# Kernel tuning notes

Hardware: AMD Instinct MI355X
Metric: run time of the kernel (lower is better)

## Reference

```python
import jax, jax.numpy as jnp
import numpy as np

DT = 0.1
WHEELBASE = 2.8
STATE_DIM = 12


def setup_inputs() -> dict:
    key = jax.random.key(0)
    k1, k2, k3 = jax.random.split(key, 3)
    b, l, h = 512, 64, 80
    x0 = jax.random.normal(k1, (b, STATE_DIM), dtype=jnp.float32)
    controls = jax.random.normal(k2, (b, l, h, 3), dtype=jnp.float32)
    deg = jax.random.uniform(k3, (b, 5), dtype=jnp.float32)
    return {"x0": x0, "controls": controls, "deg": deg}


def reference(x0, controls, deg):
    b, l, h, _ = controls.shape
    # degradation scales, broadcast over the l (candidate) dim: [b, 1]
    steer_scale = jnp.maximum(deg[:, 0:1], 0.05)
    brake_scale = jnp.maximum(deg[:, 1:2], 0.05)
    throttle_scale = jnp.maximum(deg[:, 2:3], 0.05)
    friction = jnp.maximum(deg[:, 4:5], 0.1)

    x_init = jnp.broadcast_to(x0[:, None, :], (b, l, x0.shape[-1]))  # [b,l,12]

    def step(x, u):  # x: [b,l,12], u: [b,l,3]
        delta = steer_scale * jnp.tanh(u[..., 0])
        fb = brake_scale * jax.nn.sigmoid(u[..., 1])
        fx = throttle_scale * jax.nn.sigmoid(u[..., 2])
        px, py, psi, vx, vy = (x[..., 0], x[..., 1], x[..., 2], x[..., 3], x[..., 4])
        speed = jnp.sqrt(vx * vx + vy * vy + 1e-06)
        acc = jnp.minimum(jnp.maximum(2.8 * fx - 6.5 * fb, -7.5 * friction), 3.0)
        speed2 = jnp.maximum(speed + acc * DT, 0.0)
        tan_d = jnp.tan(jnp.clip(delta, -0.75, 0.75))
        raw_yaw = speed2 / WHEELBASE * tan_d
        yaw_lim = jnp.maximum(friction * 9.81 / jnp.maximum(speed2, 2.0), 0.15)
        yaw_rate = jnp.clip(raw_yaw, -1.0, 1.0) * yaw_lim
        beta = jnp.clip(jnp.arctan(0.45 * tan_d), -0.65, 0.65)
        psi2 = psi + yaw_rate * DT
        vx2 = speed2 * jnp.cos(psi2 + beta)
        vy2 = speed2 * jnp.sin(psi2 + beta)
        px2 = px + vx2 * DT
        py2 = py + vy2 * DT
        ax = (vx2 - vx) / DT
        ay = (vy2 - vy) / DT
        x2 = jnp.stack([px2, py2, psi2, vx2, vy2, yaw_rate, ax, ay, beta, delta, fb, fx], -1)
        return x2, x2

    controls_t = jnp.moveaxis(controls, 2, 0)  # [h,b,l,3]
    _, traj = jax.lax.scan(step, x_init, controls_t)  # traj: [h,b,l,12]
    traj = jnp.concatenate([x_init[None], traj], axis=0)  # [h+1,b,l,12]
    return jnp.moveaxis(traj, 0, 2)  # [b,l,h+1,12]
```

## Files before the change

kernel.cpp:

```cpp
#include <hip/hip_runtime.h>
#include <math.h>


#define N_B 512
#define N_L 64
#define N_H 80
#define DT_F 0.1f
#define PITCH_F4 25
#define SPC 8
#define NCH 10
#define INV2PI 0.15915494309189535f

__device__ __forceinline__ float fast_rcp(float x) { return __builtin_amdgcn_rcpf(x); }

__device__ __forceinline__ float fast_tanh(float x) {
    const float e2 = __expf(2.0f * x);
    return (e2 - 1.0f) * fast_rcp(e2 + 1.0f);
}

__device__ __forceinline__ float fast_sigmoid(float x) {
    return fast_rcp(1.0f + __expf(-x));
}

__device__ __forceinline__ float fast_atan_small(float z) {
    const float z2 = z * z;
    float p = 1.0f / 9.0f;
    p = fmaf(p, z2, -1.0f / 7.0f);
    p = fmaf(p, z2, 1.0f / 5.0f);
    p = fmaf(p, z2, -1.0f / 3.0f);
    p = fmaf(p, z2, 1.0f);
    return z * p;
}

struct Ctl { float delta, fb, fx, tan_d, beta, acc; };

__device__ __forceinline__ Ctl make_ctl(float u0, float u1, float u2,
                                        float steer_scale, float brake_scale,
                                        float throttle_scale, float neg_brake_lim) {
    Ctl t;
    t.delta = steer_scale * fast_tanh(u0);
    t.fb = brake_scale    * fast_sigmoid(u1);
    t.fx = throttle_scale * fast_sigmoid(u2);
    const float dc = fminf(fmaxf(t.delta, -0.75f), 0.75f);
    const float dr = dc * INV2PI;
    const float sd = __builtin_amdgcn_sinf(dr);
    const float cd = __builtin_amdgcn_cosf(dr);
    t.tan_d = sd * fast_rcp(cd);
    t.beta = fminf(fmaxf(fast_atan_small(0.45f * t.tan_d), -0.65f), 0.65f);
    t.acc = fminf(fmaxf(2.8f * t.fx - 6.5f * t.fb, neg_brake_lim), 3.0f);
    return t;
}

__global__ __launch_bounds__(128) void degraded_bicycle_rollout_kernel(
    const float* __restrict__ x0,
    const float* __restrict__ controls,
    const float* __restrict__ deg,
    float* __restrict__ out)
{
    __shared__ float4 lds4[2][N_L * PITCH_F4];

    const int lane = threadIdx.x & 63;
    const int wave = threadIdx.x >> 6;
    const int b = blockIdx.x;

    const size_t out_b = (size_t)b * 62208;

#define FLUSH_SLICE(FBUF, FC, I0, I1)                                             \
    {                                                                             \
        const size_t obase = out_b + 12 + (size_t)(FC) * (SPC * 12);              \
        _Pragma("unroll")                                                         \
        for (int i = (I0); i < (I1); ++i) {                                       \
            const unsigned flat = i * 64 + lane;                                  \
            const unsigned l = flat / 24u;                                        \
            const unsigned q = flat - l * 24u;                                    \
            const float4 v = lds4[FBUF][l * PITCH_F4 + q];                        \
            *reinterpret_cast<float4*>(out + obase + (size_t)l * 972 + q * 4) = v;\
        }                                                                         \
    }

    if (wave == 0) {
        const float* dg = deg + b * 5;
        const float steer_scale    = fmaxf(dg[0], 0.05f);
        const float brake_scale    = fmaxf(dg[1], 0.05f);
        const float throttle_scale = fmaxf(dg[2], 0.05f);
        const float friction       = fmaxf(dg[4], 0.1f);

        const float4* x0v = reinterpret_cast<const float4*>(x0 + b * 12);
        const float4 xi0 = x0v[0];
        const float4 xi1 = x0v[1];

        float px  = xi0.x;
        float py  = xi0.y;
        float psi = xi0.z;
        float vx  = xi0.w;
        float vy  = xi1.x;

        const int tid = b * 64 + lane;
        const float4* uc = reinterpret_cast<const float4*>(controls + (size_t)tid * 240);

        const float neg_brake_lim = -7.5f * friction;
        const float yaw_num = friction * 9.81f;
        const float inv_wheelbase = 1.0f / 2.8f;

        float4 c0 = uc[0];
        float4 c1 = uc[1];
        float4 c2 = uc[2];

        for (int c = 0; c < NCH; ++c) {
            float4* lrow = &lds4[c & 1][lane * PITCH_F4];

            #pragma unroll
            for (int gg = 0; gg < 2; ++gg) {
                const int g = c * 2 + gg;
                float4 n0 = c0, n1 = c1, n2 = c2;
                if (g < 19) {
                    n0 = uc[(g + 1) * 3 + 0];
                    n1 = uc[(g + 1) * 3 + 1];
                    n2 = uc[(g + 1) * 3 + 2];
                }

                const Ctl tA = make_ctl(c0.x, c0.y, c0.z, steer_scale, brake_scale, throttle_scale, neg_brake_lim);
                const Ctl tB = make_ctl(c0.w, c1.x, c1.y, steer_scale, brake_scale, throttle_scale, neg_brake_lim);
                const Ctl tC = make_ctl(c1.z, c1.w, c2.x, steer_scale, brake_scale, throttle_scale, neg_brake_lim);
                const Ctl tD = make_ctl(c2.y, c2.z, c2.w, steer_scale, brake_scale, throttle_scale, neg_brake_lim);

#define ROLL_STEP(T, RR)                                                          \
                {                                                                 \
                    const float speed  = __builtin_amdgcn_sqrtf(fmaf(vx, vx, fmaf(vy, vy, 1e-6f))); \
                    const float speed2 = fmaxf(fmaf((T).acc, DT_F, speed), 0.0f); \
                    const float raw_yaw = speed2 * inv_wheelbase * (T).tan_d;     \
                    const float yaw_lim = fmaxf(yaw_num * fast_rcp(fmaxf(speed2, 2.0f)), 0.15f); \
                    const float yaw_rate = fminf(fmaxf(raw_yaw, -1.0f), 1.0f) * yaw_lim; \
                    const float psi2 = fmaf(yaw_rate, DT_F, psi);                 \
                    const float ang = (psi2 + (T).beta) * INV2PI;                 \
                    const float s_ = __builtin_amdgcn_sinf(ang);                  \
                    const float c_ = __builtin_amdgcn_cosf(ang);                  \
                    const float vx2 = speed2 * c_;                                \
                    const float vy2 = speed2 * s_;                                \
                    const float px2 = fmaf(vx2, DT_F, px);                        \
                    const float py2 = fmaf(vy2, DT_F, py);                        \
                    const float ax = (vx2 - vx) * 10.0f;                          \
                    const float ay = (vy2 - vy) * 10.0f;                          \
                    lrow[(RR) * 3 + 0] = make_float4(px2, py2, psi2, vx2);        \
                    lrow[(RR) * 3 + 1] = make_float4(vy2, yaw_rate, ax, ay);      \
                    lrow[(RR) * 3 + 2] = make_float4((T).beta, (T).delta, (T).fb, (T).fx); \
                    px = px2; py = py2; psi = psi2; vx = vx2; vy = vy2;           \
                }

                ROLL_STEP(tA, gg * 4 + 0)
                ROLL_STEP(tB, gg * 4 + 1)
                ROLL_STEP(tC, gg * 4 + 2)
                ROLL_STEP(tD, gg * 4 + 3)
#undef ROLL_STEP

                c0 = n0; c1 = n1; c2 = n2;
            }
            __syncthreads();
        }
    } else {
        {
            const float4* x0v = reinterpret_cast<const float4*>(x0 + b * 12);
            const float4 xq0 = x0v[0];
            const float4 xq1 = x0v[1];
            const float4 xq2 = x0v[2];
            #pragma unroll
            for (int i = 0; i < 3; ++i) {
                const unsigned flat = i * 64 + lane;
                const unsigned l = flat / 3u;
                const unsigned q = flat - l * 3u;
                const float4 v = (q == 0) ? xq0 : (q == 1) ? xq1 : xq2;
                *reinterpret_cast<float4*>(out + out_b + (size_t)l * 972 + q * 4) = v;
            }
        }
        for (int c = 0; c < NCH; ++c) {
            if (c > 0) FLUSH_SLICE((c - 1) & 1, c - 1, 0, 24)
            __syncthreads();
        }
        FLUSH_SLICE((NCH - 1) & 1, NCH - 1, 0, 24)
    }
#undef FLUSH_SLICE
}

extern "C" void kernel_launch(void* const* d_in, const int* in_sizes, int n_in,
                              void* d_out, int out_size, void* d_ws, size_t ws_size,
                              hipStream_t stream) {
    (void)in_sizes; (void)n_in; (void)d_ws; (void)ws_size; (void)out_size;
    const float* x0       = (const float*)d_in[0];
    const float* controls = (const float*)d_in[1];
    const float* deg      = (const float*)d_in[2];
    float* out            = (float*)d_out;

    dim3 grid(N_B), block(128);
    hipLaunchKernelGGL(degraded_bicycle_rollout_kernel, grid, block, 0, stream,
                       x0, controls, deg, out);
}
```

Before: 35.18 us.

## Stage controls through LDS via the flush wave with coalesced prefetch

Control inputs are no longer read per lane with strided global loads by the compute wave. The second wave now loads each chunk of controls with coalesced float4 loads into a double-buffered LDS array, one chunk ahead, alongside the output flushes. The compute wave reads its controls from LDS after the barrier. This is meant to replace uncoalesced, latency-exposed global reads on the serial compute wave. It costs extra LDS and puts more work on the flush wave, which could lengthen each barrier interval.

Measured after the change: 34.19 us. 2.8% less time.

```diff
diff --git a/kernel.cpp b/kernel.cpp
--- a/kernel.cpp
+++ b/kernel.cpp
@@ -7,6 +7,7 @@
 #define N_H 80
 #define DT_F 0.1f
 #define PITCH_F4 25
+#define CPITCH 7
 #define SPC 8
 #define NCH 10
 #define INV2PI 0.15915494309189535f
@@ -58,6 +59,7 @@
     float* __restrict__ out)
 {
     __shared__ float4 lds4[2][N_L * PITCH_F4];
+    __shared__ float4 ldsc[2][N_L * CPITCH];
 
     const int lane = threadIdx.x & 63;
     const int wave = threadIdx.x >> 6;
@@ -78,6 +80,20 @@
         }                                                                         \
     }
 
+#define LOAD_CTL(CBUF, CC)                                                        \
+    {                                                                             \
+        const size_t gbase = (size_t)b * 15360 + (size_t)(CC) * 24;               \
+        _Pragma("unroll")                                                         \
+        for (int i = 0; i < 6; ++i) {                                             \
+            const unsigned flat = i * 64 + lane;                                  \
+            const unsigned l = flat / 6u;                                         \
+            const unsigned j = flat - l * 6u;                                     \
+            const float4 v = *reinterpret_cast<const float4*>(                    \
+                controls + gbase + (size_t)l * 240 + j * 4);                      \
+            ldsc[CBUF][l * CPITCH + j] = v;                                       \
+        }                                                                         \
+    }
+
     if (wave == 0) {
         const float* dg = deg + b * 5;
         const float steer_scale    = fmaxf(dg[0], 0.05f);
@@ -95,29 +111,28 @@
         float vx  = xi0.w;
         float vy  = xi1.x;
 
-        const int tid = b * 64 + lane;
-        const float4* uc = reinterpret_cast<const float4*>(controls + (size_t)tid * 240);
-
         const float neg_brake_lim = -7.5f * friction;
         const float yaw_num = friction * 9.81f;
         const float inv_wheelbase = 1.0f / 2.8f;
 
-        float4 c0 = uc[0];
-        float4 c1 = uc[1];
-        float4 c2 = uc[2];
+        __syncthreads();
 
         for (int c = 0; c < NCH; ++c) {
             float4* lrow = &lds4[c & 1][lane * PITCH_F4];
+            const float4* crow = &ldsc[c & 1][lane * CPITCH];
+
+            const float4 u0 = crow[0];
+            const float4 u1 = crow[1];
+            const float4 u2 = crow[2];
+            const float4 u3 = crow[3];
+            const float4 u4 = crow[4];
+            const float4 u5 = crow[5];
 
             #pragma unroll
             for (int gg = 0; gg < 2; ++gg) {
-                const int g = c * 2 + gg;
-                float4 n0 = c0, n1 = c1, n2 = c2;
-                if (g < 19) {
-                    n0 = uc[(g + 1) * 3 + 0];
-                    n1 = uc[(g + 1) * 3 + 1];
-                    n2 = uc[(g + 1) * 3 + 2];
-                }
+                const float4 c0 = gg ? u3 : u0;
+                const float4 c1 = gg ? u4 : u1;
+                const float4 c2 = gg ? u5 : u2;
 
                 const Ctl tA = make_ctl(c0.x, c0.y, c0.z, steer_scale, brake_scale, throttle_scale, neg_brake_lim);
                 const Ctl tB = make_ctl(c0.w, c1.x, c1.y, steer_scale, brake_scale, throttle_scale, neg_brake_lim);
@@ -152,8 +167,6 @@
                 ROLL_STEP(tC, gg * 4 + 2)
                 ROLL_STEP(tD, gg * 4 + 3)
 #undef ROLL_STEP
-
-                c0 = n0; c1 = n1; c2 = n2;
             }
             __syncthreads();
         }
@@ -172,13 +185,18 @@
                 *reinterpret_cast<float4*>(out + out_b + (size_t)l * 972 + q * 4) = v;
             }
         }
+        LOAD_CTL(0, 0)
+        __syncthreads();
+
         for (int c = 0; c < NCH; ++c) {
             if (c > 0) FLUSH_SLICE((c - 1) & 1, c - 1, 0, 24)
+            if (c + 1 < NCH) LOAD_CTL((c + 1) & 1, c + 1)
             __syncthreads();
         }
         FLUSH_SLICE((NCH - 1) & 1, NCH - 1, 0, 24)
     }
 #undef FLUSH_SLICE
+#undef LOAD_CTL
 }
 
 extern "C" void kernel_launch(void* const* d_in, const int* in_sizes, int n_in,
```

## Enlarge LDS chunks, add flush waves, polynomial tan, and simplify speed recurrence

Applied to the files above, without the earlier changes.

Chunks grow from 8 to 20 timesteps (4 chunks instead of 10), and the block grows to 256 threads so three waves split the writeback of each chunk while one wave integrates. tan of the clamped steering angle becomes an odd polynomial instead of hardware sin/cos plus a reciprocal. Speed is carried as sqrt(s2^2+eps), using the fact that the new velocity's magnitude equals s2, which removes the dependency on vx/vy. The LDS footprint grows to about 125KB per block, which likely limits each CU to one block and serialises the 512 blocks. The truncated tan series also adds small approximation error near the clamp limit.

Measured after the change: 43.90 us. 1.25x slower.

```diff
diff --git a/kernel.cpp b/kernel.cpp
--- a/kernel.cpp
+++ b/kernel.cpp
@@ -6,9 +6,9 @@
 #define N_L 64
 #define N_H 80
 #define DT_F 0.1f
-#define PITCH_F4 25
-#define SPC 8
-#define NCH 10
+#define PITCH_F4 61
+#define SPC 20
+#define NCH 4
 #define INV2PI 0.15915494309189535f
 
 __device__ __forceinline__ float fast_rcp(float x) { return __builtin_amdgcn_rcpf(x); }
@@ -32,6 +32,17 @@
     return z * p;
 }
 
+__device__ __forceinline__ float fast_tan_075(float x) {
+    const float x2 = x * x;
+    float p = 0.0035916f;
+    p = fmaf(p, x2, 0.0088632f);
+    p = fmaf(p, x2, 0.0218695f);
+    p = fmaf(p, x2, 0.0539683f);
+    p = fmaf(p, x2, 0.1333333f);
+    p = fmaf(p, x2, 0.3333333f);
+    return fmaf(p * x2, x, x);
+}
+
 struct Ctl { float delta, fb, fx, tan_d, beta, acc; };
 
 __device__ __forceinline__ Ctl make_ctl(float u0, float u1, float u2,
@@ -42,16 +53,13 @@
     t.fb = brake_scale    * fast_sigmoid(u1);
     t.fx = throttle_scale * fast_sigmoid(u2);
     const float dc = fminf(fmaxf(t.delta, -0.75f), 0.75f);
-    const float dr = dc * INV2PI;
-    const float sd = __builtin_amdgcn_sinf(dr);
-    const float cd = __builtin_amdgcn_cosf(dr);
-    t.tan_d = sd * fast_rcp(cd);
+    t.tan_d = fast_tan_075(dc);
     t.beta = fminf(fmaxf(fast_atan_small(0.45f * t.tan_d), -0.65f), 0.65f);
     t.acc = fminf(fmaxf(2.8f * t.fx - 6.5f * t.fb, neg_brake_lim), 3.0f);
     return t;
 }
 
-__global__ __launch_bounds__(128) void degraded_bicycle_rollout_kernel(
+__global__ __launch_bounds__(256) void degraded_bicycle_rollout_kernel(
     const float* __restrict__ x0,
     const float* __restrict__ controls,
     const float* __restrict__ deg,
@@ -60,7 +68,7 @@
     __shared__ float4 lds4[2][N_L * PITCH_F4];
 
     const int lane = threadIdx.x & 63;
-    const int wave = threadIdx.x >> 6;
+    const int wv   = threadIdx.x >> 6;
     const int b = blockIdx.x;
 
     const size_t out_b = (size_t)b * 62208;
@@ -71,14 +79,14 @@
         _Pragma("unroll")                                                         \
         for (int i = (I0); i < (I1); ++i) {                                       \
             const unsigned flat = i * 64 + lane;                                  \
-            const unsigned l = flat / 24u;                                        \
-            const unsigned q = flat - l * 24u;                                    \
+            const unsigned l = flat / 60u;                                        \
+            const unsigned q = flat - l * 60u;                                    \
             const float4 v = lds4[FBUF][l * PITCH_F4 + q];                        \
             *reinterpret_cast<float4*>(out + obase + (size_t)l * 972 + q * 4) = v;\
         }                                                                         \
     }
 
-    if (wave == 0) {
+    if (wv == 0) {
         const float* dg = deg + b * 5;
         const float steer_scale    = fmaxf(dg[0], 0.05f);
         const float brake_scale    = fmaxf(dg[1], 0.05f);
@@ -92,16 +100,17 @@
         float px  = xi0.x;
         float py  = xi0.y;
         float psi = xi0.z;
-        float vx  = xi0.w;
-        float vy  = xi1.x;
-
-        const int tid = b * 64 + lane;
-        const float4* uc = reinterpret_cast<const float4*>(controls + (size_t)tid * 240);
+        float vxp = xi0.w;
+        float vyp = xi1.x;
+        float s = __builtin_amdgcn_sqrtf(fmaf(vxp, vxp, fmaf(vyp, vyp, 1e-6f)));
 
         const float neg_brake_lim = -7.5f * friction;
         const float yaw_num = friction * 9.81f;
         const float inv_wheelbase = 1.0f / 2.8f;
 
+        const int tid = b * 64 + lane;
+        const float4* uc = reinterpret_cast<const float4*>(controls + (size_t)tid * 240);
+
         float4 c0 = uc[0];
         float4 c1 = uc[1];
         float4 c2 = uc[2];
@@ -110,8 +119,8 @@
             float4* lrow = &lds4[c & 1][lane * PITCH_F4];
 
             #pragma unroll
-            for (int gg = 0; gg < 2; ++gg) {
-                const int g = c * 2 + gg;
+            for (int gg = 0; gg < 5; ++gg) {
+                const int g = c * 5 + gg;
                 float4 n0 = c0, n1 = c1, n2 = c2;
                 if (g < 19) {
                     n0 = uc[(g + 1) * 3 + 0];
@@ -126,25 +135,25 @@
 
 #define ROLL_STEP(T, RR)                                                          \
                 {                                                                 \
-                    const float speed  = __builtin_amdgcn_sqrtf(fmaf(vx, vx, fmaf(vy, vy, 1e-6f))); \
-                    const float speed2 = fmaxf(fmaf((T).acc, DT_F, speed), 0.0f); \
-                    const float raw_yaw = speed2 * inv_wheelbase * (T).tan_d;     \
-                    const float yaw_lim = fmaxf(yaw_num * fast_rcp(fmaxf(speed2, 2.0f)), 0.15f); \
+                    const float s2 = fmaxf(fmaf((T).acc, DT_F, s), 0.0f);         \
+                    const float raw_yaw = s2 * inv_wheelbase * (T).tan_d;         \
+                    const float yaw_lim = fmaxf(yaw_num * fast_rcp(fmaxf(s2, 2.0f)), 0.15f); \
                     const float yaw_rate = fminf(fmaxf(raw_yaw, -1.0f), 1.0f) * yaw_lim; \
                     const float psi2 = fmaf(yaw_rate, DT_F, psi);                 \
                     const float ang = (psi2 + (T).beta) * INV2PI;                 \
-                    const float s_ = __builtin_amdgcn_sinf(ang);                  \
-                    const float c_ = __builtin_amdgcn_cosf(ang);                  \
-                    const float vx2 = speed2 * c_;                                \
-                    const float vy2 = speed2 * s_;                                \
+                    const float sn = __builtin_amdgcn_sinf(ang);                  \
+                    const float cs = __builtin_amdgcn_cosf(ang);                  \
+                    const float vx2 = s2 * cs;                                    \
+                    const float vy2 = s2 * sn;                                    \
                     const float px2 = fmaf(vx2, DT_F, px);                        \
                     const float py2 = fmaf(vy2, DT_F, py);                        \
-                    const float ax = (vx2 - vx) * 10.0f;                          \
-                    const float ay = (vy2 - vy) * 10.0f;                          \
+                    const float ax = (vx2 - vxp) * 10.0f;                         \
+                    const float ay = (vy2 - vyp) * 10.0f;                         \
                     lrow[(RR) * 3 + 0] = make_float4(px2, py2, psi2, vx2);        \
                     lrow[(RR) * 3 + 1] = make_float4(vy2, yaw_rate, ax, ay);      \
                     lrow[(RR) * 3 + 2] = make_float4((T).beta, (T).delta, (T).fb, (T).fx); \
-                    px = px2; py = py2; psi = psi2; vx = vx2; vy = vy2;           \
+                    s = __builtin_amdgcn_sqrtf(fmaf(s2, s2, 1e-6f));              \
+                    px = px2; py = py2; psi = psi2; vxp = vx2; vyp = vy2;         \
                 }
 
                 ROLL_STEP(tA, gg * 4 + 0)
@@ -158,7 +167,8 @@
             __syncthreads();
         }
     } else {
-        {
+        const int i0 = (wv - 1) * 20;
+        if (wv == 2) {
             const float4* x0v = reinterpret_cast<const float4*>(x0 + b * 12);
             const float4 xq0 = x0v[0];
             const float4 xq1 = x0v[1];
@@ -172,11 +182,15 @@
                 *reinterpret_cast<float4*>(out + out_b + (size_t)l * 972 + q * 4) = v;
             }
         }
+
         for (int c = 0; c < NCH; ++c) {
-            if (c > 0) FLUSH_SLICE((c - 1) & 1, c - 1, 0, 24)
             __syncthreads();
+            if (c + 1 < NCH) {
+                FLUSH_SLICE(c & 1, c, i0, i0 + 20)
+            } else {
+                FLUSH_SLICE(c & 1, c, i0, i0 + 20)
+            }
         }
-        FLUSH_SLICE((NCH - 1) & 1, NCH - 1, 0, 24)
     }
 #undef FLUSH_SLICE
 }
@@ -190,7 +204,7 @@
     const float* deg      = (const float*)d_in[2];
     float* out            = (float*)d_out;
 
-    dim3 grid(N_B), block(128);
+    dim3 grid(N_B), block(256);
     hipLaunchKernelGGL(degraded_bicycle_rollout_kernel, grid, block, 0, stream,
                        x0, controls, deg, out);
 }
```
